# Kernel optimization log

Measured on AMD Instinct MI355X. Metric: run time of the kernel, lower is better.

## Reference

```python
import jax, jax.numpy as jnp
import numpy as np

INPUT_SIZE = 24
HIDDEN = 128
N_LAYERS = 2
OUT_SIZE = 1


def setup_inputs() -> dict:
    key = jax.random.key(0)
    ks = jax.random.split(key, 2 + 4 * N_LAYERS + 2)
    x = jax.random.normal(ks[0], (2048, 128, INPUT_SIZE), dtype=jnp.float32)
    params = {}
    s = 1.0 / np.sqrt(HIDDEN)
    idx = 1
    for l in range(N_LAYERS):
        in_dim = INPUT_SIZE if l == 0 else HIDDEN
        params[f"W_ih{l}"] = jax.random.uniform(ks[idx], (4 * HIDDEN, in_dim), minval=-s, maxval=s, dtype=jnp.float32); idx += 1
        params[f"W_hh{l}"] = jax.random.uniform(ks[idx], (4 * HIDDEN, HIDDEN), minval=-s, maxval=s, dtype=jnp.float32); idx += 1
        params[f"b_ih{l}"] = jax.random.uniform(ks[idx], (4 * HIDDEN,), minval=-s, maxval=s, dtype=jnp.float32); idx += 1
        params[f"b_hh{l}"] = jax.random.uniform(ks[idx], (4 * HIDDEN,), minval=-s, maxval=s, dtype=jnp.float32); idx += 1
    params["W_fc"] = jax.random.uniform(ks[idx], (OUT_SIZE, HIDDEN), minval=-s, maxval=s, dtype=jnp.float32); idx += 1
    params["b_fc"] = jax.random.uniform(ks[idx], (OUT_SIZE,), minval=-s, maxval=s, dtype=jnp.float32)
    return {"x": x, **params}


def _lstm_layer(x, W_ih, W_hh, b_ih, b_hh):
    # x: [B, T, in] -> outputs [B, T, H]. PyTorch gate order: i, f, g, o.
    B = x.shape[0]
    H = W_hh.shape[1]
    # precompute input projections for all timesteps: [T, B, 4H]
    xproj = jnp.einsum('bti,gi->tbg', x, W_ih) + b_ih + b_hh

    def step(carry, xp_t):
        h, c = carry
        gates = xp_t + h @ W_hh.T  # [B, 4H]
        i, f, g, o = jnp.split(gates, 4, axis=-1)
        i = jax.nn.sigmoid(i)
        f = jax.nn.sigmoid(f)
        g = jnp.tanh(g)
        o = jax.nn.sigmoid(o)
        c = f * c + i * g
        h = o * jnp.tanh(c)
        return (h, c), h

    h0 = jnp.zeros((B, H), dtype=x.dtype)
    c0 = jnp.zeros((B, H), dtype=x.dtype)
    (_, _), hs = jax.lax.scan(step, (h0, c0), xproj)
    return jnp.transpose(hs, (1, 0, 2))  # [B, T, H]


def reference(x, W_ih0, W_hh0, b_ih0, b_hh0, W_ih1, W_hh1, b_ih1, b_hh1, W_fc, b_fc):
    # Inference-mode forward: inter-layer dropout (p=0.2) is identity in eval.
    h1 = _lstm_layer(x, W_ih0, W_hh0, b_ih0, b_hh0)   # [B, T, H]
    h2 = _lstm_layer(h1, W_ih1, W_hh1, b_ih1, b_hh1)  # [B, T, H]
    last = h2[:, -1, :]                               # [B, H]
    return last @ W_fc.T + b_fc                       # [B, 1]
```

## Files before the change

### kernel.cpp

```cpp
#include <hip/hip_runtime.h>

#define TSTEPS 128
#define NIN 24
#define HD 128
#define BT 16
#define NBLK 128
#define NTH 512

#define RS    136
#define SLOT  (BT*RS)
#define H1B   (2*SLOT)
#define W1B   (4*SLOT)
#define SM_ELTS (W1B + 65536)
#define SM_BYTES (SM_ELTS*2)

#define XH_ROW 32
#define XH_BYTES ((size_t)2048 * TSTEPS * XH_ROW * 2)

typedef _Float16 half8  __attribute__((ext_vector_type(8)));
typedef _Float16 half4v __attribute__((ext_vector_type(4)));
typedef float    floatx4 __attribute__((ext_vector_type(4)));

__device__ __forceinline__ float sigf(float x) {
    return __builtin_amdgcn_rcpf(1.0f + __expf(-x));
}
__device__ __forceinline__ float tanh_f(float x) {
    return 1.0f - 2.0f * __builtin_amdgcn_rcpf(1.0f + __expf(2.0f * x));
}

__device__ __forceinline__ half8 ldw8(const float* p) {
    const float4* q = (const float4*)p;
    float4 a = q[0], b = q[1];
    half8 r;
    r[0] = (_Float16)a.x; r[1] = (_Float16)a.y; r[2] = (_Float16)a.z; r[3] = (_Float16)a.w;
    r[4] = (_Float16)b.x; r[5] = (_Float16)b.y; r[6] = (_Float16)b.z; r[7] = (_Float16)b.w;
    return r;
}

__device__ __forceinline__ void barrier_lgkm() {
    asm volatile("s_waitcnt lgkmcnt(0)" ::: "memory");
    __builtin_amdgcn_s_barrier();
    __builtin_amdgcn_sched_barrier(0);
}

__global__ __launch_bounds__(256)
void xcvt(const float* __restrict__ x, _Float16* __restrict__ xh)
{
    int c = blockIdx.x * 256 + threadIdx.x;
    if (c >= 2048 * TSTEPS * 4) return;
    int part = c & 3;
    size_t row = (size_t)(c >> 2);
    half8 v;
    if (part < 3) {
        v = ldw8(x + row * NIN + part * 8);
    } else {
        v = (half8){0, 0, 0, 0, 0, 0, 0, 0};
        v[0] = (_Float16)1.0f;
    }
    *(half8*)&xh[c * (size_t)8] = v;
}

template<int MODE>
__global__ __launch_bounds__(NTH, 2)
void lstm2_fused(const float* __restrict__ x,
                 const float* __restrict__ Wih0, const float* __restrict__ Whh0,
                 const float* __restrict__ bih0, const float* __restrict__ bhh0,
                 const float* __restrict__ Wih1, const float* __restrict__ Whh1,
                 const float* __restrict__ bih1, const float* __restrict__ bhh1,
                 const float* __restrict__ Wfc,  const float* __restrict__ bfc,
                 float* __restrict__ out, const _Float16* __restrict__ xh)
{
    extern __shared__ __align__(16) _Float16 SM[];

    const int tid = threadIdx.x;
    const int blk = blockIdx.x;
    const int wv  = tid >> 6;
    const int ln  = tid & 63;
    const int qd  = ln >> 4;
    const int nn  = ln & 15;
    const int b0  = blk * BT;
    const int hcol = wv * 16 + qd * 4;

    const half8 z8 = {0, 0, 0, 0, 0, 0, 0, 0};
    const floatx4 zf4 = {0.f, 0.f, 0.f, 0.f};

    for (int i = tid * 8; i < W1B; i += NTH * 8) *(half8*)&SM[i] = z8;

    floatx4 bias1[4];
#pragma unroll
    for (int tI = 0; tI < 4; ++tI)
#pragma unroll
        for (int r = 0; r < 4; ++r)
            bias1[tI][r] = bih1[tI * HD + hcol + r] + bhh1[tI * HD + hcol + r];

    half8 wih0[4];
    half8 whh0[4][4], wih1[4][4];
#pragma unroll
    for (int tI = 0; tI < 4; ++tI) {
        int g = tI * HD + wv * 16 + nn;
        if (qd < 3) {
            wih0[tI] = ldw8(Wih0 + g * NIN + qd * 8);
        } else {
            wih0[tI] = z8;
            wih0[tI][0] = (_Float16)(bih0[g] + bhh0[g]);
        }
#pragma unroll
        for (int kk = 0; kk < 4; ++kk) {
            whh0[tI][kk] = ldw8(Whh0 + g * HD + kk * 32 + qd * 8);
            wih1[tI][kk] = ldw8(Wih1 + g * HD + kk * 32 + qd * 8);
        }
    }

    for (int i = tid; i < 512 * 32; i += NTH) {
        int g  = i >> 5;
        int k0 = (i & 31) << 2;
        float4 v = *(const float4*)(Whh1 + g * HD + k0);
        half4v h; h[0] = (_Float16)v.x; h[1] = (_Float16)v.y;
                  h[2] = (_Float16)v.z; h[3] = (_Float16)v.w;
        int dst = W1B + ((((g >> 4) & 7) * 16) + (g >> 7) * 4 + (k0 >> 5)) * 512
                      + (((k0 >> 3) & 3) * 16 + (g & 15)) * 8 + (k0 & 7);
        *(half4v*)&SM[dst] = h;
    }
    const int w1base = W1B + wv * 8192 + ln * 8;

    const _Float16* xbase = nullptr;
    const float*    xrow  = nullptr;
    half8 ax, axn;
    float4 pf0, pf1;
    if constexpr (MODE == 0) {
        xbase = xh + ((size_t)(b0 + nn) * TSTEPS) * XH_ROW + qd * 8;
        ax = *(const half8*)(xbase);
    } else {
        xrow = x + (size_t)(b0 + nn) * (TSTEPS * NIN) + (qd < 3 ? qd * 8 : 0);
        pf0 = *(const float4*)(xrow);
        pf1 = *(const float4*)(xrow + 4);
    }

    float cs0[4] = {0.f, 0.f, 0.f, 0.f};
    float cs1[4] = {0.f, 0.f, 0.f, 0.f};

    __syncthreads();

    {
        if constexpr (MODE == 1) {
            if (qd < 3) {
                ax = z8;
                ax[0] = (_Float16)pf0.x; ax[1] = (_Float16)pf0.y; ax[2] = (_Float16)pf0.z; ax[3] = (_Float16)pf0.w;
                ax[4] = (_Float16)pf1.x; ax[5] = (_Float16)pf1.y; ax[6] = (_Float16)pf1.z; ax[7] = (_Float16)pf1.w;
            } else {
                ax = z8; ax[0] = (_Float16)1.0f;
            }
            pf0 = *(const float4*)(xrow + NIN);
            pf1 = *(const float4*)(xrow + NIN + 4);
        } else {
            axn = *(const half8*)(xbase + XH_ROW);
        }

        floatx4 acc0[4];
#pragma unroll
        for (int tI = 0; tI < 4; ++tI)
            acc0[tI] = __builtin_amdgcn_mfma_f32_16x16x32_f16(wih0[tI], ax, zf4, 0, 0, 0);

        half4v hw;
#pragma unroll
        for (int r = 0; r < 4; ++r) {
            float iv = sigf(acc0[0][r]);
            float gv = tanh_f(acc0[2][r]);
            float ov = sigf(acc0[3][r]);
            float cn = iv * gv;
            cs0[r] = cn;
            hw[r] = (_Float16)(ov * tanh_f(cn));
        }
        *(half4v*)&SM[0 * SLOT + nn * RS + hcol] = hw;
        if constexpr (MODE == 0) ax = axn;
    }

#pragma unroll 1
    for (int t = 1; t < TSTEPS; ++t) {
        barrier_lgkm();

        if constexpr (MODE == 0) {
            const int tn = (t < TSTEPS - 1) ? t + 1 : TSTEPS - 1;
            axn = *(const half8*)(xbase + (size_t)tn * XH_ROW);
        } else {
            if (qd < 3) {
                ax = z8;
                ax[0] = (_Float16)pf0.x; ax[1] = (_Float16)pf0.y; ax[2] = (_Float16)pf0.z; ax[3] = (_Float16)pf0.w;
                ax[4] = (_Float16)pf1.x; ax[5] = (_Float16)pf1.y; ax[6] = (_Float16)pf1.z; ax[7] = (_Float16)pf1.w;
            } else {
                ax = z8; ax[0] = (_Float16)1.0f;
            }
            const int tn = (t < TSTEPS - 1) ? t + 1 : TSTEPS - 1;
            pf0 = *(const float4*)(xrow + (size_t)tn * NIN);
            pf1 = *(const float4*)(xrow + (size_t)tn * NIN + 4);
        }

        const int h0r = ((t - 1) & 1) * SLOT;
        const int h0w = (t & 1) * SLOT;
        const int h1r = H1B + (t & 1) * SLOT;
        const int h1w = H1B + ((t & 1) ^ 1) * SLOT;

        floatx4 acc0[4], acc1[4];
#pragma unroll
        for (int tI = 0; tI < 4; ++tI) {
            acc0[tI] = __builtin_amdgcn_mfma_f32_16x16x32_f16(wih0[tI], ax, zf4, 0, 0, 0);
            acc1[tI] = bias1[tI];
        }

        __builtin_amdgcn_s_setprio(1);
#pragma unroll
        for (int kk = 0; kk < 4; ++kk) {
            const half8 ah = *(const half8*)&SM[h0r + nn * RS + kk * 32 + qd * 8];
#pragma unroll
            for (int tI = 0; tI < 4; ++tI)
                acc0[tI] = __builtin_amdgcn_mfma_f32_16x16x32_f16(whh0[tI][kk], ah, acc0[tI], 0, 0, 0);
#pragma unroll
            for (int tI = 0; tI < 4; ++tI)
                acc1[tI] = __builtin_amdgcn_mfma_f32_16x16x32_f16(wih1[tI][kk], ah, acc1[tI], 0, 0, 0);
        }
#pragma unroll
        for (int kk = 0; kk < 4; ++kk) {
            const half8 a2 = *(const half8*)&SM[h1r + nn * RS + kk * 32 + qd * 8];
#pragma unroll
            for (int tI = 0; tI < 4; ++tI) {
                const half8 w1 = *(const half8*)&SM[w1base + (tI * 4 + kk) * 512];
                acc1[tI] = __builtin_amdgcn_mfma_f32_16x16x32_f16(w1, a2, acc1[tI], 0, 0, 0);
            }
        }
        __builtin_amdgcn_s_setprio(0);

        {
            half4v hw;
#pragma unroll
            for (int r = 0; r < 4; ++r) {
                float iv = sigf(acc0[0][r]);
                float fv = sigf(acc0[1][r]);
                float gv = tanh_f(acc0[2][r]);
                float ov = sigf(acc0[3][r]);
                float cn = fv * cs0[r] + iv * gv;
                cs0[r] = cn;
                hw[r] = (_Float16)(ov * tanh_f(cn));
            }
            *(half4v*)&SM[h0w + nn * RS + hcol] = hw;
        }
        {
            half4v hw;
#pragma unroll
            for (int r = 0; r < 4; ++r) {
                float iv = sigf(acc1[0][r]);
                float fv = sigf(acc1[1][r]);
                float gv = tanh_f(acc1[2][r]);
                float ov = sigf(acc1[3][r]);
                float cn = fv * cs1[r] + iv * gv;
                cs1[r] = cn;
                hw[r] = (_Float16)(ov * tanh_f(cn));
            }
            *(half4v*)&SM[h1w + nn * RS + hcol] = hw;
        }
        if constexpr (MODE == 0) ax = axn;
    }

    {
        barrier_lgkm();
        floatx4 acc1[4];
#pragma unroll
        for (int tI = 0; tI < 4; ++tI) acc1[tI] = bias1[tI];

#pragma unroll
        for (int kk = 0; kk < 4; ++kk) {
            const half8 ah = *(const half8*)&SM[SLOT + nn * RS + kk * 32 + qd * 8];
#pragma unroll
            for (int tI = 0; tI < 4; ++tI)
                acc1[tI] = __builtin_amdgcn_mfma_f32_16x16x32_f16(wih1[tI][kk], ah, acc1[tI], 0, 0, 0);
        }
#pragma unroll
        for (int kk = 0; kk < 4; ++kk) {
            const half8 a2 = *(const half8*)&SM[H1B + nn * RS + kk * 32 + qd * 8];
#pragma unroll
            for (int tI = 0; tI < 4; ++tI) {
                const half8 w1 = *(const half8*)&SM[w1base + (tI * 4 + kk) * 512];
                acc1[tI] = __builtin_amdgcn_mfma_f32_16x16x32_f16(w1, a2, acc1[tI], 0, 0, 0);
            }
        }

        half4v hw;
#pragma unroll
        for (int r = 0; r < 4; ++r) {
            float iv = sigf(acc1[0][r]);
            float fv = sigf(acc1[1][r]);
            float gv = tanh_f(acc1[2][r]);
            float ov = sigf(acc1[3][r]);
            float cn = fv * cs1[r] + iv * gv;
            hw[r] = (_Float16)(ov * tanh_f(cn));
        }
        *(half4v*)&SM[H1B + SLOT + nn * RS + hcol] = hw;
    }
    barrier_lgkm();

    {
        int b = tid >> 5, sub = tid & 31;
        const _Float16* hp = &SM[H1B + SLOT + b * RS + sub * 4];
        const float4 wv4 = *(const float4*)(Wfc + sub * 4);
        float s = (float)hp[0] * wv4.x + (float)hp[1] * wv4.y
                + (float)hp[2] * wv4.z + (float)hp[3] * wv4.w;
        s += __shfl_down(s, 16, 32);
        s += __shfl_down(s, 8, 32);
        s += __shfl_down(s, 4, 32);
        s += __shfl_down(s, 2, 32);
        s += __shfl_down(s, 1, 32);
        if (sub == 0) out[b0 + b] = s + bfc[0];
    }
}

extern "C" void kernel_launch(void* const* d_in, const int* in_sizes, int n_in,
                              void* d_out, int out_size, void* d_ws, size_t ws_size,
                              hipStream_t stream) {
    static bool attr_set = false;
    if (!attr_set) {
        hipFuncSetAttribute(reinterpret_cast<const void*>(&lstm2_fused<0>),
                            hipFuncAttributeMaxDynamicSharedMemorySize, SM_BYTES);
        hipFuncSetAttribute(reinterpret_cast<const void*>(&lstm2_fused<1>),
                            hipFuncAttributeMaxDynamicSharedMemorySize, SM_BYTES);
        attr_set = true;
    }
    const float* x    = (const float*)d_in[0];
    const float* Wih0 = (const float*)d_in[1];
    const float* Whh0 = (const float*)d_in[2];
    const float* bih0 = (const float*)d_in[3];
    const float* bhh0 = (const float*)d_in[4];
    const float* Wih1 = (const float*)d_in[5];
    const float* Whh1 = (const float*)d_in[6];
    const float* bih1 = (const float*)d_in[7];
    const float* bhh1 = (const float*)d_in[8];
    const float* Wfc  = (const float*)d_in[9];
    const float* bfc  = (const float*)d_in[10];
    float* out = (float*)d_out;

    if (ws_size >= XH_BYTES) {
        _Float16* xhp = (_Float16*)d_ws;
        xcvt<<<dim3((2048 * TSTEPS * 4 + 255) / 256), dim3(256), 0, stream>>>(x, xhp);
        lstm2_fused<0><<<dim3(NBLK), dim3(NTH), SM_BYTES, stream>>>(
            x, Wih0, Whh0, bih0, bhh0, Wih1, Whh1, bih1, bhh1, Wfc, bfc, out, xhp);
    } else {
        lstm2_fused<1><<<dim3(NBLK), dim3(NTH), SM_BYTES, stream>>>(
            x, Wih0, Whh0, bih0, bhh0, Wih1, Whh1, bih1, bhh1, Wfc, bfc, out, nullptr);
    }
}
```

Measured before the change: 344.3 us.

## Split LSTM layers across two wave groups in a 1024-thread block

Doubles the block to 16 waves: waves 0-7 compute layer 0 and waves 8-15 compute layer 1 concurrently, wavefront-pipelined through shared memory with barriers each step. It also drops the separate fp16 x-conversion pre-kernel and always reads fp32 x directly. The aim is to shorten each step's critical path by running the two layers' MFMA chains in parallel and to remove the extra kernel launch. In exchange each barrier now synchronises 16 waves, and per-thread register pressure must fit the stated launch bounds.

```diff
diff --git a/kernel.cpp b/kernel.cpp
--- a/kernel.cpp
+++ b/kernel.cpp
@@ -5,7 +5,7 @@
 #define HD 128
 #define BT 16
 #define NBLK 128
-#define NTH 512
+#define NTH 1024
 
 #define RS    136
 #define SLOT  (BT*RS)
@@ -13,9 +13,6 @@
 #define W1B   (4*SLOT)
 #define SM_ELTS (W1B + 65536)
 #define SM_BYTES (SM_ELTS*2)
-
-#define XH_ROW 32
-#define XH_BYTES ((size_t)2048 * TSTEPS * XH_ROW * 2)
 
 typedef _Float16 half8  __attribute__((ext_vector_type(8)));
 typedef _Float16 half4v __attribute__((ext_vector_type(4)));
@@ -43,32 +40,14 @@
     __builtin_amdgcn_sched_barrier(0);
 }
 
-__global__ __launch_bounds__(256)
-void xcvt(const float* __restrict__ x, _Float16* __restrict__ xh)
-{
-    int c = blockIdx.x * 256 + threadIdx.x;
-    if (c >= 2048 * TSTEPS * 4) return;
-    int part = c & 3;
-    size_t row = (size_t)(c >> 2);
-    half8 v;
-    if (part < 3) {
-        v = ldw8(x + row * NIN + part * 8);
-    } else {
-        v = (half8){0, 0, 0, 0, 0, 0, 0, 0};
-        v[0] = (_Float16)1.0f;
-    }
-    *(half8*)&xh[c * (size_t)8] = v;
-}
-
-template<int MODE>
-__global__ __launch_bounds__(NTH, 2)
+__global__ __launch_bounds__(NTH, 4)
 void lstm2_fused(const float* __restrict__ x,
                  const float* __restrict__ Wih0, const float* __restrict__ Whh0,
                  const float* __restrict__ bih0, const float* __restrict__ bhh0,
                  const float* __restrict__ Wih1, const float* __restrict__ Whh1,
                  const float* __restrict__ bih1, const float* __restrict__ bhh1,
                  const float* __restrict__ Wfc,  const float* __restrict__ bfc,
-                 float* __restrict__ out, const _Float16* __restrict__ xh)
+                 float* __restrict__ out)
 {
     extern __shared__ __align__(16) _Float16 SM[];
 
@@ -79,38 +58,11 @@
     const int qd  = ln >> 4;
     const int nn  = ln & 15;
     const int b0  = blk * BT;
-    const int hcol = wv * 16 + qd * 4;
 
     const half8 z8 = {0, 0, 0, 0, 0, 0, 0, 0};
     const floatx4 zf4 = {0.f, 0.f, 0.f, 0.f};
 
     for (int i = tid * 8; i < W1B; i += NTH * 8) *(half8*)&SM[i] = z8;
-
-    floatx4 bias1[4];
-#pragma unroll
-    for (int tI = 0; tI < 4; ++tI)
-#pragma unroll
-        for (int r = 0; r < 4; ++r)
-            bias1[tI][r] = bih1[tI * HD + hcol + r] + bhh1[tI * HD + hcol + r];
-
-    half8 wih0[4];
-    half8 whh0[4][4], wih1[4][4];
-#pragma unroll
-    for (int tI = 0; tI < 4; ++tI) {
-        int g = tI * HD + wv * 16 + nn;
-        if (qd < 3) {
-            wih0[tI] = ldw8(Wih0 + g * NIN + qd * 8);
-        } else {
-            wih0[tI] = z8;
-            wih0[tI][0] = (_Float16)(bih0[g] + bhh0[g]);
-        }
-#pragma unroll
-        for (int kk = 0; kk < 4; ++kk) {
-            whh0[tI][kk] = ldw8(Whh0 + g * HD + kk * 32 + qd * 8);
-            wih1[tI][kk] = ldw8(Wih1 + g * HD + kk * 32 + qd * 8);
-        }
-    }
-
     for (int i = tid; i < 512 * 32; i += NTH) {
         int g  = i >> 5;
         int k0 = (i & 31) << 2;
@@ -121,30 +73,38 @@
                       + (((k0 >> 3) & 3) * 16 + (g & 15)) * 8 + (k0 & 7);
         *(half4v*)&SM[dst] = h;
     }
-    const int w1base = W1B + wv * 8192 + ln * 8;
-
-    const _Float16* xbase = nullptr;
-    const float*    xrow  = nullptr;
-    half8 ax, axn;
-    float4 pf0, pf1;
-    if constexpr (MODE == 0) {
-        xbase = xh + ((size_t)(b0 + nn) * TSTEPS) * XH_ROW + qd * 8;
-        ax = *(const half8*)(xbase);
-    } else {
-        xrow = x + (size_t)(b0 + nn) * (TSTEPS * NIN) + (qd < 3 ? qd * 8 : 0);
-        pf0 = *(const float4*)(xrow);
-        pf1 = *(const float4*)(xrow + 4);
-    }
-
-    float cs0[4] = {0.f, 0.f, 0.f, 0.f};
-    float cs1[4] = {0.f, 0.f, 0.f, 0.f};
-
-    __syncthreads();
-
-    {
-        if constexpr (MODE == 1) {
+
+    if (wv < 8) {
+        const int hw_  = wv;
+        const int hcol = hw_ * 16 + qd * 4;
+
+        half8 wih0[4];
+        half8 whh0[4][4];
+#pragma unroll
+        for (int tI = 0; tI < 4; ++tI) {
+            int g = tI * HD + hw_ * 16 + nn;
             if (qd < 3) {
-                ax = z8;
+                wih0[tI] = ldw8(Wih0 + g * NIN + qd * 8);
+            } else {
+                wih0[tI] = z8;
+                wih0[tI][0] = (_Float16)(bih0[g] + bhh0[g]);
+            }
+#pragma unroll
+            for (int kk = 0; kk < 4; ++kk)
+                whh0[tI][kk] = ldw8(Whh0 + g * HD + kk * 32 + qd * 8);
+        }
+
+        const float* xrow = x + (size_t)(b0 + nn) * (TSTEPS * NIN) + (qd < 3 ? qd * 8 : 0);
+        float4 pf0 = *(const float4*)(xrow);
+        float4 pf1 = *(const float4*)(xrow + 4);
+
+        float cs0[4] = {0.f, 0.f, 0.f, 0.f};
+
+        __syncthreads();
+
+        {
+            half8 ax;
+            if (qd < 3) {
                 ax[0] = (_Float16)pf0.x; ax[1] = (_Float16)pf0.y; ax[2] = (_Float16)pf0.z; ax[3] = (_Float16)pf0.w;
                 ax[4] = (_Float16)pf1.x; ax[5] = (_Float16)pf1.y; ax[6] = (_Float16)pf1.z; ax[7] = (_Float16)pf1.w;
             } else {
@@ -152,84 +112,60 @@
             }
             pf0 = *(const float4*)(xrow + NIN);
             pf1 = *(const float4*)(xrow + NIN + 4);
-        } else {
-            axn = *(const half8*)(xbase + XH_ROW);
-        }
-
-        floatx4 acc0[4];
-#pragma unroll
-        for (int tI = 0; tI < 4; ++tI)
-            acc0[tI] = __builtin_amdgcn_mfma_f32_16x16x32_f16(wih0[tI], ax, zf4, 0, 0, 0);
-
-        half4v hw;
-#pragma unroll
-        for (int r = 0; r < 4; ++r) {
-            float iv = sigf(acc0[0][r]);
-            float gv = tanh_f(acc0[2][r]);
-            float ov = sigf(acc0[3][r]);
-            float cn = iv * gv;
-            cs0[r] = cn;
-            hw[r] = (_Float16)(ov * tanh_f(cn));
-        }
-        *(half4v*)&SM[0 * SLOT + nn * RS + hcol] = hw;
-        if constexpr (MODE == 0) ax = axn;
-    }
+
+            floatx4 acc0[4];
+#pragma unroll
+            for (int tI = 0; tI < 4; ++tI)
+                acc0[tI] = __builtin_amdgcn_mfma_f32_16x16x32_f16(wih0[tI], ax, zf4, 0, 0, 0);
+
+            half4v hw;
+#pragma unroll
+            for (int r = 0; r < 4; ++r) {
+                float iv = sigf(acc0[0][r]);
+                float gv = tanh_f(acc0[2][r]);
+                float ov = sigf(acc0[3][r]);
+                float cn = iv * gv;
+                cs0[r] = cn;
+                hw[r] = (_Float16)(ov * tanh_f(cn));
+            }
+            *(half4v*)&SM[0 * SLOT + nn * RS + hcol] = hw;
+        }
 
 #pragma unroll 1
-    for (int t = 1; t < TSTEPS; ++t) {
-        barrier_lgkm();
-
-        if constexpr (MODE == 0) {
-            const int tn = (t < TSTEPS - 1) ? t + 1 : TSTEPS - 1;
-            axn = *(const half8*)(xbase + (size_t)tn * XH_ROW);
-        } else {
+        for (int t = 1; t < TSTEPS; ++t) {
+            barrier_lgkm();
+
+            half8 ax;
             if (qd < 3) {
-                ax = z8;
                 ax[0] = (_Float16)pf0.x; ax[1] = (_Float16)pf0.y; ax[2] = (_Float16)pf0.z; ax[3] = (_Float16)pf0.w;
                 ax[4] = (_Float16)pf1.x; ax[5] = (_Float16)pf1.y; ax[6] = (_Float16)pf1.z; ax[7] = (_Float16)pf1.w;
             } else {
                 ax = z8; ax[0] = (_Float16)1.0f;
             }
-            const int tn = (t < TSTEPS - 1) ? t + 1 : TSTEPS - 1;
-            pf0 = *(const float4*)(xrow + (size_t)tn * NIN);
-            pf1 = *(const float4*)(xrow + (size_t)tn * NIN + 4);
-        }
-
-        const int h0r = ((t - 1) & 1) * SLOT;
-        const int h0w = (t & 1) * SLOT;
-        const int h1r = H1B + (t & 1) * SLOT;
-        const int h1w = H1B + ((t & 1) ^ 1) * SLOT;
-
-        floatx4 acc0[4], acc1[4];
-#pragma unroll
-        for (int tI = 0; tI < 4; ++tI) {
-            acc0[tI] = __builtin_amdgcn_mfma_f32_16x16x32_f16(wih0[tI], ax, zf4, 0, 0, 0);
-            acc1[tI] = bias1[tI];
-        }
-
-        __builtin_amdgcn_s_setprio(1);
-#pragma unroll
-        for (int kk = 0; kk < 4; ++kk) {
-            const half8 ah = *(const half8*)&SM[h0r + nn * RS + kk * 32 + qd * 8];
+            {
+                const int tn = (t < TSTEPS - 1) ? t + 1 : TSTEPS - 1;
+                pf0 = *(const float4*)(xrow + (size_t)tn * NIN);
+                pf1 = *(const float4*)(xrow + (size_t)tn * NIN + 4);
+            }
+
+            const int h0r = ((t - 1) & 1) * SLOT;
+            const int h0w = (t & 1) * SLOT;
+
+            floatx4 acc0[4];
 #pragma unroll
             for (int tI = 0; tI < 4; ++tI)
-                acc0[tI] = __builtin_amdgcn_mfma_f32_16x16x32_f16(whh0[tI][kk], ah, acc0[tI], 0, 0, 0);
-#pragma unroll
-            for (int tI = 0; tI < 4; ++tI)
-                acc1[tI] = __builtin_amdgcn_mfma_f32_16x16x32_f16(wih1[tI][kk], ah, acc1[tI], 0, 0, 0);
-        }
-#pragma unroll
-        for (int kk = 0; kk < 4; ++kk) {
-            const half8 a2 = *(const half8*)&SM[h1r + nn * RS + kk * 32 + qd * 8];
-#pragma unroll
-            for (int tI = 0; tI < 4; ++tI) {
-                const half8 w1 = *(const half8*)&SM[w1base + (tI * 4 + kk) * 512];
-                acc1[tI] = __builtin_amdgcn_mfma_f32_16x16x32_f16(w1, a2, acc1[tI], 0, 0, 0);
-            }
-        }
-        __builtin_amdgcn_s_setprio(0);
-
-        {
+                acc0[tI] = __builtin_amdgcn_mfma_f32_16x16x32_f16(wih0[tI], ax, zf4, 0, 0, 0);
+
+            __builtin_amdgcn_s_setprio(1);
+#pragma unroll
+            for (int kk = 0; kk < 4; ++kk) {
+                const half8 ah = *(const half8*)&SM[h0r + nn * RS + kk * 32 + qd * 8];
+#pragma unroll
+                for (int tI = 0; tI < 4; ++tI)
+                    acc0[tI] = __builtin_amdgcn_mfma_f32_16x16x32_f16(whh0[tI][kk], ah, acc0[tI], 0, 0, 0);
+            }
+            __builtin_amdgcn_s_setprio(0);
+
             half4v hw;
 #pragma unroll
             for (int r = 0; r < 4; ++r) {
@@ -243,7 +179,62 @@
             }
             *(half4v*)&SM[h0w + nn * RS + hcol] = hw;
         }
-        {
+
+        barrier_lgkm();
+        barrier_lgkm();
+    } else {
+        const int hw_  = wv - 8;
+        const int hcol = hw_ * 16 + qd * 4;
+
+        floatx4 bias1[4];
+        half8 wih1[4][4];
+#pragma unroll
+        for (int tI = 0; tI < 4; ++tI) {
+#pragma unroll
+            for (int r = 0; r < 4; ++r)
+                bias1[tI][r] = bih1[tI * HD + hcol + r] + bhh1[tI * HD + hcol + r];
+            int g = tI * HD + hw_ * 16 + nn;
+#pragma unroll
+            for (int kk = 0; kk < 4; ++kk)
+                wih1[tI][kk] = ldw8(Wih1 + g * HD + kk * 32 + qd * 8);
+        }
+        const int w1base = W1B + hw_ * 8192 + ln * 8;
+
+        float cs1[4] = {0.f, 0.f, 0.f, 0.f};
+
+        __syncthreads();
+
+#pragma unroll 1
+        for (int t = 1; t < TSTEPS; ++t) {
+            barrier_lgkm();
+
+            const int h0r = ((t - 1) & 1) * SLOT;
+            const int h1r = H1B + (t & 1) * SLOT;
+            const int h1w = H1B + ((t & 1) ^ 1) * SLOT;
+
+            floatx4 acc1[4];
+#pragma unroll
+            for (int tI = 0; tI < 4; ++tI) acc1[tI] = bias1[tI];
+
+            __builtin_amdgcn_s_setprio(1);
+#pragma unroll
+            for (int kk = 0; kk < 4; ++kk) {
+                const half8 ah = *(const half8*)&SM[h0r + nn * RS + kk * 32 + qd * 8];
+#pragma unroll
+                for (int tI = 0; tI < 4; ++tI)
+                    acc1[tI] = __builtin_amdgcn_mfma_f32_16x16x32_f16(wih1[tI][kk], ah, acc1[tI], 0, 0, 0);
+            }
+#pragma unroll
+            for (int kk = 0; kk < 4; ++kk) {
+                const half8 a2 = *(const half8*)&SM[h1r + nn * RS + kk * 32 + qd * 8];
+#pragma unroll
+                for (int tI = 0; tI < 4; ++tI) {
+                    const half8 w1 = *(const half8*)&SM[w1base + (tI * 4 + kk) * 512];
+                    acc1[tI] = __builtin_amdgcn_mfma_f32_16x16x32_f16(w1, a2, acc1[tI], 0, 0, 0);
+                }
+            }
+            __builtin_amdgcn_s_setprio(0);
+
             half4v hw;
 #pragma unroll
             for (int r = 0; r < 4; ++r) {
@@ -257,47 +248,44 @@
             }
             *(half4v*)&SM[h1w + nn * RS + hcol] = hw;
         }
-        if constexpr (MODE == 0) ax = axn;
+
+        barrier_lgkm();
+        {
+            floatx4 acc1[4];
+#pragma unroll
+            for (int tI = 0; tI < 4; ++tI) acc1[tI] = bias1[tI];
+#pragma unroll
+            for (int kk = 0; kk < 4; ++kk) {
+                const half8 ah = *(const half8*)&SM[SLOT + nn * RS + kk * 32 + qd * 8];
+#pragma unroll
+                for (int tI = 0; tI < 4; ++tI)
+                    acc1[tI] = __builtin_amdgcn_mfma_f32_16x16x32_f16(wih1[tI][kk], ah, acc1[tI], 0, 0, 0);
+            }
+#pragma unroll
+            for (int kk = 0; kk < 4; ++kk) {
+                const half8 a2 = *(const half8*)&SM[H1B + nn * RS + kk * 32 + qd * 8];
+#pragma unroll
+                for (int tI = 0; tI < 4; ++tI) {
+                    const half8 w1 = *(const half8*)&SM[w1base + (tI * 4 + kk) * 512];
+                    acc1[tI] = __builtin_amdgcn_mfma_f32_16x16x32_f16(w1, a2, acc1[tI], 0, 0, 0);
+                }
+            }
+            half4v hw;
+#pragma unroll
+            for (int r = 0; r < 4; ++r) {
+                float iv = sigf(acc1[0][r]);
+                float fv = sigf(acc1[1][r]);
+                float gv = tanh_f(acc1[2][r]);
+                float ov = sigf(acc1[3][r]);
+                float cn = fv * cs1[r] + iv * gv;
+                hw[r] = (_Float16)(ov * tanh_f(cn));
+            }
+            *(half4v*)&SM[H1B + SLOT + nn * RS + hcol] = hw;
+        }
+        barrier_lgkm();
     }
 
-    {
-        barrier_lgkm();
-        floatx4 acc1[4];
-#pragma unroll
-        for (int tI = 0; tI < 4; ++tI) acc1[tI] = bias1[tI];
-
-#pragma unroll
-        for (int kk = 0; kk < 4; ++kk) {
-            const half8 ah = *(const half8*)&SM[SLOT + nn * RS + kk * 32 + qd * 8];
-#pragma unroll
-            for (int tI = 0; tI < 4; ++tI)
-                acc1[tI] = __builtin_amdgcn_mfma_f32_16x16x32_f16(wih1[tI][kk], ah, acc1[tI], 0, 0, 0);
-        }
-#pragma unroll
-        for (int kk = 0; kk < 4; ++kk) {
-            const half8 a2 = *(const half8*)&SM[H1B + nn * RS + kk * 32 + qd * 8];
-#pragma unroll
-            for (int tI = 0; tI < 4; ++tI) {
-                const half8 w1 = *(const half8*)&SM[w1base + (tI * 4 + kk) * 512];
-                acc1[tI] = __builtin_amdgcn_mfma_f32_16x16x32_f16(w1, a2, acc1[tI], 0, 0, 0);
-            }
-        }
-
-        half4v hw;
-#pragma unroll
-        for (int r = 0; r < 4; ++r) {
-            float iv = sigf(acc1[0][r]);
-            float fv = sigf(acc1[1][r]);
-            float gv = tanh_f(acc1[2][r]);
-            float ov = sigf(acc1[3][r]);
-            float cn = fv * cs1[r] + iv * gv;
-            hw[r] = (_Float16)(ov * tanh_f(cn));
-        }
-        *(half4v*)&SM[H1B + SLOT + nn * RS + hcol] = hw;
-    }
-    barrier_lgkm();
-
-    {
+    if (tid < 512) {
         int b = tid >> 5, sub = tid & 31;
         const _Float16* hp = &SM[H1B + SLOT + b * RS + sub * 4];
         const float4 wv4 = *(const float4*)(Wfc + sub * 4);
@@ -317,9 +305,7 @@
                               hipStream_t stream) {
     static bool attr_set = false;
     if (!attr_set) {
-        hipFuncSetAttribute(reinterpret_cast<const void*>(&lstm2_fused<0>),
-                            hipFuncAttributeMaxDynamicSharedMemorySize, SM_BYTES);
-        hipFuncSetAttribute(reinterpret_cast<const void*>(&lstm2_fused<1>),
+        hipFuncSetAttribute(reinterpret_cast<const void*>(&lstm2_fused),
                             hipFuncAttributeMaxDynamicSharedMemorySize, SM_BYTES);
         attr_set = true;
     }
@@ -336,13 +322,6 @@
     const float* bfc  = (const float*)d_in[10];
     float* out = (float*)d_out;
 
-    if (ws_size >= XH_BYTES) {
-        _Float16* xhp = (_Float16*)d_ws;
-        xcvt<<<dim3((2048 * TSTEPS * 4 + 255) / 256), dim3(256), 0, stream>>>(x, xhp);
-        lstm2_fused<0><<<dim3(NBLK), dim3(NTH), SM_BYTES, stream>>>(
-            x, Wih0, Whh0, bih0, bhh0, Wih1, Whh1, bih1, bhh1, Wfc, bfc, out, xhp);
-    } else {
-        lstm2_fused<1><<<dim3(NBLK), dim3(NTH), SM_BYTES, stream>>>(
-            x, Wih0, Whh0, bih0, bhh0, Wih1, Whh1, bih1, bhh1, Wfc, bfc, out, nullptr);
-    }
-}
+    lstm2_fused<<<dim3(NBLK), dim3(NTH), SM_BYTES, stream>>>(
+        x, Wih0, Whh0, bih0, bhh0, Wih1, Whh1, bih1, bhh1, Wfc, bfc, out);
+}
```

After: 319.6 us, median of 2. 7.2% less time.
